# Optimization experiments

Measured on AMD Instinct MI355X. Metric: run time of the kernel, lower is better.

## Reference

```python
import jax, jax.numpy as jnp
import numpy as np

# --- constants mirroring init_kwargs ---
DIM = 1024
N_HEADS = 16
N_KV_HEADS = 4
HEAD_DIM = DIM // N_HEADS          # 64
REP = N_HEADS // N_KV_HEADS        # 4
ROPE_THETA = 10000.0
WINDOW = 512
N_GLOBAL = 64
EPS = 1e-6


def setup_inputs() -> dict:
    key = jax.random.key(0)
    ks = jax.random.split(key, 7)
    B, L = 2, 2048
    x = jax.random.normal(ks[0], (B, L, DIM), dtype=jnp.float32)
    s = 0.02
    wq = jax.random.normal(ks[1], (DIM, N_HEADS * HEAD_DIM), dtype=jnp.float32) * s
    wk = jax.random.normal(ks[2], (DIM, N_KV_HEADS * HEAD_DIM), dtype=jnp.float32) * s
    wv = jax.random.normal(ks[3], (DIM, N_KV_HEADS * HEAD_DIM), dtype=jnp.float32) * s
    wo = jax.random.normal(ks[4], (N_HEADS * HEAD_DIM, DIM), dtype=jnp.float32) * s
    gq = jnp.ones((HEAD_DIM,), dtype=jnp.float32) + 0.01 * jax.random.normal(ks[5], (HEAD_DIM,), dtype=jnp.float32)
    gk = jnp.ones((HEAD_DIM,), dtype=jnp.float32) + 0.01 * jax.random.normal(ks[6], (HEAD_DIM,), dtype=jnp.float32)
    return {"x": x, "wq": wq, "wk": wk, "wv": wv, "wo": wo, "gq": gq, "gk": gk}


def _rmsnorm(t, g):
    # QKNorm: RMS norm over head_dim with learnable per-dim scale
    return t * jax.lax.rsqrt(jnp.mean(t * t, axis=-1, keepdims=True) + EPS) * g


def _rope(t, cos, sin):
    # t: [B,H,L,hd]; complex RoPE over consecutive pairs (2i, 2i+1)
    t1 = t[..., 0::2]
    t2 = t[..., 1::2]
    o1 = t1 * cos - t2 * sin
    o2 = t1 * sin + t2 * cos
    return jnp.stack([o1, o2], axis=-1).reshape(t.shape)


def reference(x, wq, wk, wv, wo, gq, gk):
    B, L, D = x.shape
    q = (x @ wq).reshape(B, L, N_HEADS, HEAD_DIM)
    k = (x @ wk).reshape(B, L, N_KV_HEADS, HEAD_DIM)
    v = (x @ wv).reshape(B, L, N_KV_HEADS, HEAD_DIM)
    q = _rmsnorm(q, gq)
    k = _rmsnorm(k, gk)
    q = q.transpose(0, 2, 1, 3)  # [B,H,L,hd]
    k = k.transpose(0, 2, 1, 3)
    v = v.transpose(0, 2, 1, 3)

    # RoPE frequencies (start_pos = 0)
    inv_freq = 1.0 / (ROPE_THETA ** (jnp.arange(0, HEAD_DIM, 2, dtype=jnp.float32) / HEAD_DIM))
    ang = jnp.arange(L, dtype=jnp.float32)[:, None] * inv_freq[None, :]  # [L, hd/2]
    cos, sin = jnp.cos(ang), jnp.sin(ang)
    q = _rope(q, cos, sin)
    k = _rope(k, cos, sin)

    # GQA: repeat kv heads (repeat_interleave on head dim)
    k = jnp.repeat(k, REP, axis=1)
    v = jnp.repeat(v, REP, axis=1)

    scores = jnp.einsum("bhqd,bhkd->bhqk", q, k) / np.sqrt(HEAD_DIM).astype(np.float32)

    # sliding-window + global-token causal mask
    half = WINDOW // 2
    i = jnp.arange(L)[:, None]
    j = jnp.arange(L)[None, :]
    m = (j <= i) & ((j >= i - half) | (j < N_GLOBAL))  # [L,L] bool
    scores = jnp.where(m[None, None], scores, -jnp.inf)

    attn = jax.nn.softmax(scores.astype(jnp.float32), axis=-1).astype(scores.dtype)
    out = jnp.einsum("bhqk,bhkd->bhqd", attn, v)
    out = out.transpose(0, 2, 1, 3).reshape(B, L, N_HEADS * HEAD_DIM)
    return out @ wo
```

## Files before the change

kernel.cpp:

```cpp
#include <hip/hip_runtime.h>
#include <hip/hip_bf16.h>

typedef __bf16 bf16x8 __attribute__((ext_vector_type(8)));
typedef __bf16 bf16x4 __attribute__((ext_vector_type(4)));
typedef float  f32x4  __attribute__((ext_vector_type(4)));
typedef short  s16x4  __attribute__((ext_vector_type(4)));

__device__ __forceinline__ __bf16 to_bf16(float f) {
    __hip_bfloat16 h = __float2bfloat16(f);
    return *reinterpret_cast<__bf16*>(&h);
}

__device__ __forceinline__ f32x4 mfma32(bf16x8 a, bf16x8 b, f32x4 c) {
    return __builtin_amdgcn_mfma_f32_16x16x32_bf16(a, b, c, 0, 0, 0);
}
__device__ __forceinline__ f32x4 mfma16(bf16x4 a, bf16x4 b, f32x4 c) {
#if __has_builtin(__builtin_amdgcn_mfma_f32_16x16x16_bf16)
    return __builtin_amdgcn_mfma_f32_16x16x16_bf16(a, b, c, 0, 0, 0);
#else
    return __builtin_amdgcn_mfma_f32_16x16x16bf16_1k(
        __builtin_bit_cast(s16x4, a), __builtin_bit_cast(s16x4, b), c, 0, 0, 0);
#endif
}

__device__ __forceinline__ void gload_lds16(const __bf16* g, __bf16* l) {
    __builtin_amdgcn_global_load_lds(
        (const __attribute__((address_space(1))) void*)g,
        (__attribute__((address_space(3))) void*)l, 16, 0, 0);
}


__global__ __launch_bounds__(256) void prep_k(const float* __restrict__ wq,
                                              const float* __restrict__ wk,
                                              const float* __restrict__ wv,
                                              __bf16* __restrict__ WqkvT,
                                              float2* __restrict__ rope_tab) {
    int b = blockIdx.x, tid = threadIdx.x;
    if (b >= 1536) {
        int idx = (b - 1536) * 256 + tid;
        int pos = idx >> 5, f = idx & 31;
        float ex = (float)(2 * f) * (1.0f / 64.0f);
        float invf = expf(-ex * 9.210340371976184f);
        float ang = (float)pos * invf;
        rope_tab[idx] = make_float2(cosf(ang), sinf(ang));
        return;
    }
    __shared__ float tile[32][36];
    const float* src; __bf16* dst; int N, idx;
    if (b < 1024)      { src = wq; dst = WqkvT;                        N = 1024; idx = b; }
    else if (b < 1280) { src = wk; dst = WqkvT + (size_t)1024 * 1024;  N = 256;  idx = b - 1024; }
    else               { src = wv; dst = WqkvT + (size_t)1280 * 1024;  N = 256;  idx = b - 1280; }
    int k0 = (idx & 31) * 32, n0 = (idx >> 5) * 32;
    int row = tid >> 3, c4 = tid & 7;
    *(f32x4*)&tile[row][c4 * 4] = *(const f32x4*)(src + (size_t)(k0 + row) * N + n0 + c4 * 4);
    __syncthreads();
    bf16x4 v;
#pragma unroll
    for (int j = 0; j < 4; ++j) v[j] = to_bf16(tile[c4 * 4 + j][row]);
    *(bf16x4*)&dst[(size_t)(n0 + row) * 1024 + k0 + c4 * 4] = v;
}

__global__ __launch_bounds__(512, 4) void gemmqkv_k(const float* __restrict__ X,
                                                    const __bf16* __restrict__ BT,
                                                    const float2* __restrict__ rope_tab,
                                                    const float* __restrict__ gq,
                                                    const float* __restrict__ gk,
                                                    const float* __restrict__ wo,
                                                    __bf16* __restrict__ Qb,
                                                    __bf16* __restrict__ Kbl,
                                                    __bf16* __restrict__ Vt,
                                                    __bf16* __restrict__ WoT) {
    extern __shared__ char smem_raw[];
    int tid = threadIdx.x;
    if (blockIdx.y >= 12) {
        float* scr = (float*)smem_raw;
        int bidT = (blockIdx.y - 12) * 32 + blockIdx.x;
        int sub = tid >> 8, t8 = tid & 255;
        int row = t8 >> 3, c4 = t8 & 7;
        float* my = scr + sub * 1152;
#pragma unroll
        for (int r = 0; r < 4; ++r) {
            int tile = bidT * 8 + r * 2 + sub;
            int k0 = (tile & 31) * 32, n0t = (tile >> 5) * 32;
            __syncthreads();
            *(f32x4*)&my[row * 36 + c4 * 4] =
                *(const f32x4*)(wo + (size_t)(k0 + row) * 1024 + n0t + c4 * 4);
            __syncthreads();
            bf16x4 v;
#pragma unroll
            for (int j = 0; j < 4; ++j) v[j] = to_bf16(my[(c4 * 4 + j) * 36 + row]);
            *(bf16x4*)&WoT[(size_t)(n0t + row) * 1024 + k0 + c4 * 4] = v;
        }
        return;
    }
    __shared__ float ssp[4][128];
    __bf16* smem = (__bf16*)smem_raw;
    int m0 = blockIdx.x * 128, n0 = blockIdx.y * 128;
    int wid = tid >> 6, lane = tid & 63;
    int wm = (wid & 1) * 64, wn = (wid >> 1) * 32;
    int lm = lane & 15, qd = lane >> 4;
    int arow = tid >> 3, aslot = tid & 7;
    int asrc = aslot ^ (arow & 7);
    f32x4 acc[4][2] = {};
    f32x4 areg[4];

    auto A_LOAD = [&](int t) {
        const float* ap = X + (size_t)(m0 + arow) * 1024 + t * 64 + asrc * 8;
        areg[0] = *(const f32x4*)ap;
        areg[1] = *(const f32x4*)(ap + 4);
        const float* ap2 = ap + (size_t)64 * 1024;
        areg[2] = *(const f32x4*)ap2;
        areg[3] = *(const f32x4*)(ap2 + 4);
    };
    auto A_WRITE = [&](int bsel) {
        __bf16* ab = smem + bsel * 16384;
        bf16x8 w0, w1;
#pragma unroll
        for (int j = 0; j < 4; ++j) {
            w0[j] = to_bf16(areg[0][j]); w0[4 + j] = to_bf16(areg[1][j]);
            w1[j] = to_bf16(areg[2][j]); w1[4 + j] = to_bf16(areg[3][j]);
        }
        *(bf16x8*)&ab[arow * 64 + aslot * 8] = w0;
        *(bf16x8*)&ab[(arow + 64) * 64 + aslot * 8] = w1;
    };
    auto B_GLOAD = [&](int bsel, int t) {
        __bf16* base = smem + bsel * 16384 + 8192;
#pragma unroll
        for (int r = 0; r < 2; ++r) {
            int row = r * 64 + (tid >> 3);
            int c8 = (tid & 7) ^ (row & 7);
            gload_lds16(BT + (size_t)(n0 + row) * 1024 + t * 64 + c8 * 8,
                        base + r * 4096 + wid * 512);
        }
    };

    A_LOAD(0);
    B_GLOAD(0, 0);
    asm volatile("s_waitcnt vmcnt(2)" ::: "memory");
    A_WRITE(0);

    for (int t = 0; t < 16; ++t) {
        if (t + 1 < 16) {
            A_LOAD(t + 1);
            B_GLOAD((t + 1) & 1, t + 1);
            asm volatile("s_waitcnt vmcnt(6)" ::: "memory");
        } else {
            asm volatile("s_waitcnt vmcnt(0)" ::: "memory");
        }
        asm volatile("s_waitcnt lgkmcnt(0)" ::: "memory");
        __builtin_amdgcn_s_barrier();
        __builtin_amdgcn_sched_barrier(0);
        const __bf16* cA = smem + (t & 1) * 16384;
        const __bf16* cB = cA + 8192;
#pragma unroll
        for (int kh = 0; kh < 2; ++kh) {
            bf16x8 af[4], bfr[2];
#pragma unroll
            for (int t4 = 0; t4 < 4; ++t4) {
                int row = wm + t4 * 16 + lm;
                af[t4] = *(const bf16x8*)&cA[row * 64 + (((kh * 4 + qd) ^ (row & 7)) * 8)];
            }
#pragma unroll
            for (int j = 0; j < 2; ++j) {
                int col = wn + j * 16 + lm;
                bfr[j] = *(const bf16x8*)&cB[col * 64 + (((kh * 4 + qd) ^ (col & 7)) * 8)];
            }
#pragma unroll
            for (int ti = 0; ti < 4; ++ti)
#pragma unroll
                for (int tj = 0; tj < 2; ++tj)
                    acc[ti][tj] = mfma32(af[ti], bfr[tj], acc[ti][tj]);
        }
        if (t + 1 < 16) {
            asm volatile("s_waitcnt vmcnt(2)" ::: "memory");
            A_WRITE((t + 1) & 1);
        }
        asm volatile("s_waitcnt lgkmcnt(0)" ::: "memory");
        __builtin_amdgcn_s_barrier();
    }

    int head0 = n0 >> 6;
    int quad = wid >> 1;
    int chead = wn & 63;

    if (head0 < 20) {
        int head = head0 + (quad >> 1);
        bool isq = head < 16;
        const float* gvec = isq ? gq : gk;
        float gam[2];
#pragma unroll
        for (int tj = 0; tj < 2; ++tj) gam[tj] = gvec[chead + tj * 16 + lm];

#pragma unroll
        for (int ti = 0; ti < 4; ++ti)
#pragma unroll
            for (int r = 0; r < 4; ++r) {
                float sq = acc[ti][0][r] * acc[ti][0][r] + acc[ti][1][r] * acc[ti][1][r];
                sq += __shfl_xor(sq, 1);
                sq += __shfl_xor(sq, 2);
                sq += __shfl_xor(sq, 4);
                sq += __shfl_xor(sq, 8);
                if (lm == 0) ssp[quad][wm + ti * 16 + qd * 4 + r] = sq;
            }
        __syncthreads();

#pragma unroll
        for (int ti = 0; ti < 4; ++ti)
#pragma unroll
            for (int r = 0; r < 4; ++r) {
                int row = wm + ti * 16 + qd * 4 + r;
                int t = m0 + row;
                int pos = t & 2047, bb = t >> 11;
                float ss = ssp[quad][row] + ssp[quad ^ 1][row];
                float scale = rsqrtf(ss * (1.0f / 64.0f) + 1e-6f);
#pragma unroll
                for (int tj = 0; tj < 2; ++tj) {
                    int cw = chead + tj * 16 + lm;
                    float v = acc[ti][tj][r] * scale * gam[tj];
                    float2 cs = rope_tab[pos * 32 + (cw >> 1)];
                    float pv = __shfl_xor(v, 1);
                    float outv = (cw & 1) ? (pv * cs.y + v * cs.x) : (v * cs.x - pv * cs.y);
                    if (isq) {
                        int kvh = head >> 2, h4 = head & 3;
                        size_t off = (((((size_t)bb * 4 + kvh) * 128 + (pos >> 4)) * 4 + h4) * 16
                                      + (pos & 15)) * 64 + cw;
                        Qb[off] = to_bf16(outv * 0.125f);
                    } else {
                        int kvg = head - 16;
                        Kbl[(((size_t)bb * 4 + kvg) * 2048 + pos) * 64 + cw] = to_bf16(outv);
                    }
                }
            }
    } else {
        __bf16* tvh = smem + (quad >> 1) * 8704;
        int bb = m0 >> 11, pos0 = m0 & 2047;
#pragma unroll
        for (int ti = 0; ti < 4; ++ti)
#pragma unroll
            for (int tj = 0; tj < 2; ++tj)
#pragma unroll
                for (int r = 0; r < 4; ++r) {
                    int row = wm + ti * 16 + qd * 4 + r;
                    int cw = chead + tj * 16 + lm;
                    tvh[cw * 136 + row] = to_bf16(acc[ti][tj][r]);
                }
        __syncthreads();
        int hh = tid >> 8, t8 = tid & 255;
        int kvg = head0 + hh - 20;
        size_t gg = (size_t)bb * 4 + kvg;
        const __bf16* tvr = smem + hh * 8704;
#pragma unroll
        for (int p = 0; p < 4; ++p) {
            int d = p * 16 + (t8 >> 4);
            int tok = (t8 & 15) * 8;
            bf16x8 vvv = *(const bf16x8*)&tvr[d * 136 + tok];
            *(bf16x8*)(Vt + (gg * 64 + d) * 2048 + pos0 + tok) = vvv;
        }
    }
}

__global__ __launch_bounds__(512, 4) void gemm_op_k(const __bf16* __restrict__ A,
                                                    const __bf16* __restrict__ BT,
                                                    float* __restrict__ C) {
    extern __shared__ char smem_raw[];
    __bf16* smem = (__bf16*)smem_raw;
    int tid = threadIdx.x;
    int m0 = blockIdx.x * 128, n0 = blockIdx.y * 64;
    int wid = tid >> 6, lane = tid & 63;
    int wm = (wid & 3) * 32, wn = (wid >> 2) * 32;
    int lm = lane & 15, qd = lane >> 4;
    f32x4 acc[2][2] = {};
    auto STAGE = [&](int bsel, int t) {
        __bf16* base = smem + bsel * 12288;
#pragma unroll
        for (int r = 0; r < 2; ++r) {
            int row = r * 64 + (tid >> 3);
            int c8 = (tid & 7) ^ (row & 7);
            gload_lds16(A + (size_t)(m0 + row) * 1024 + t * 64 + c8 * 8,
                        base + r * 4096 + wid * 512);
        }
        {
            int row = tid >> 3;
            int c8 = (tid & 7) ^ (row & 7);
            gload_lds16(BT + (size_t)(n0 + row) * 1024 + t * 64 + c8 * 8,
                        base + 8192 + wid * 512);
        }
    };
    STAGE(0, 0);
    for (int t = 0; t < 16; ++t) {
        if (t + 1 < 16) {
            STAGE((t + 1) & 1, t + 1);
            asm volatile("s_waitcnt vmcnt(3)" ::: "memory");
        } else {
            asm volatile("s_waitcnt vmcnt(0)" ::: "memory");
        }
        __builtin_amdgcn_s_barrier();
        __builtin_amdgcn_sched_barrier(0);
        const __bf16* cA = smem + (t & 1) * 12288;
        const __bf16* cB = cA + 8192;
#pragma unroll
        for (int kh = 0; kh < 2; ++kh) {
            bf16x8 af[2], bfr[2];
#pragma unroll
            for (int i = 0; i < 2; ++i) {
                int row = wm + i * 16 + lm;
                af[i] = *(const bf16x8*)&cA[row * 64 + (((kh * 4 + qd) ^ (row & 7)) * 8)];
                int col = wn + i * 16 + lm;
                bfr[i] = *(const bf16x8*)&cB[col * 64 + (((kh * 4 + qd) ^ (col & 7)) * 8)];
            }
#pragma unroll
            for (int ti = 0; ti < 2; ++ti)
#pragma unroll
                for (int tj = 0; tj < 2; ++tj)
                    acc[ti][tj] = mfma32(af[ti], bfr[tj], acc[ti][tj]);
        }
        asm volatile("s_waitcnt lgkmcnt(0)" ::: "memory");
        __builtin_amdgcn_s_barrier();
    }
#pragma unroll
    for (int ti = 0; ti < 2; ++ti)
#pragma unroll
        for (int tj = 0; tj < 2; ++tj)
#pragma unroll
            for (int r = 0; r < 4; ++r) {
                int row = m0 + wm + ti * 16 + qd * 4 + r;
                int col = n0 + wn + tj * 16 + lm;
                C[(size_t)row * 1024 + col] = acc[ti][tj][r];
            }
}

__global__ __launch_bounds__(512, 4) void attn_k(const __bf16* __restrict__ Qb,
                                                 const __bf16* __restrict__ Kbl,
                                                 const __bf16* __restrict__ Vt,
                                                 __bf16* __restrict__ aout) {
    __shared__ __bf16 Kt[2][64 * 64];
    __shared__ __bf16 Vl[2][64 * 64];
    int tid = threadIdx.x, wid = tid >> 6, lane = tid & 63;
    int l15 = lane & 15, quad = lane >> 4;
    int qb = blockIdx.x, kvh = blockIdx.y, b = blockIdx.z;
    int qg = wid >> 2;
    int h4 = wid & 3;
    int iw0 = qb * 32;
    int iw = iw0 + qg * 16;
    int g = b * 4 + kvh;
    int h = kvh * 4 + h4;
    int e7 = l15 & 7;

    int qbi = qb * 2 + qg;
    const __bf16* qp = Qb + ((((size_t)g * 128 + qbi) * 4 + h4) * 16 + l15) * 64 + quad * 8;
    bf16x8 qf0 = *(const bf16x8*)qp;
    bf16x8 qf1 = *(const bf16x8*)(qp + 32);

    int ts = (iw0 - 256) >> 6; if (ts < 1) ts = 1;
    int tmaxb = (iw0 + 31) >> 6;
    int n_all = (tmaxb >= ts) ? (tmaxb - ts + 2) : 1;
    int tmaxw = (iw + 15) >> 6;

    const __bf16* Kg = Kbl + (size_t)g * 2048 * 64;
    const __bf16* Vg = Vt + (size_t)g * 64 * 2048;

    int r0 = tid >> 3, c0 = tid & 7;
    int kl = r0 * 64 + ((c0 ^ (r0 & 7)) * 8);

    bf16x8 kr, vr;
    auto stage_load = [&](int tt) {
        kr = *(const bf16x8*)(Kg + (size_t)tt * 64 * 64 + r0 * 64 + c0 * 8);
        vr = *(const bf16x8*)(Vg + (size_t)r0 * 2048 + tt * 64 + c0 * 8);
    };
    auto stage_write = [&](int buf) {
        *(bf16x8*)&Kt[buf][kl] = kr;
        *(bf16x8*)&Vl[buf][kl] = vr;
    };

    stage_load(0);
    stage_write(0);

    f32x4 o[4] = {};
    float mr = -1e30f, lrp = 0.f;
    int iq = iw + l15;

    for (int idx = 0; idx < n_all; ++idx) {
        int tt = (idx == 0) ? 0 : ts + idx - 1;
        if (idx + 1 < n_all) stage_load(ts + idx);
        __syncthreads();
        int buf = idx & 1;

        f32x4 s[4] = {};
#pragma unroll
        for (int nt = 0; nt < 4; ++nt) {
            const __bf16* kp = &Kt[buf][(nt * 16 + l15) * 64];
            bf16x8 k0 = *(const bf16x8*)(kp + ((quad ^ e7) * 8));
            bf16x8 k1 = *(const bf16x8*)(kp + (((quad + 4) ^ e7) * 8));
            s[nt] = mfma32(k0, qf0, s[nt]);
            s[nt] = mfma32(k1, qf1, s[nt]);
        }

        bool need_mask = (tt >= tmaxw) || (tt >= 1 && tt * 64 < iw + 15 - 256);
        if (need_mask) {
#pragma unroll
            for (int nt = 0; nt < 4; ++nt)
#pragma unroll
                for (int r = 0; r < 4; ++r) {
                    int j = tt * 64 + nt * 16 + quad * 4 + r;
                    bool valid = (j <= iq) && ((j >= iq - 256) || (j < 64));
                    s[nt][r] = valid ? s[nt][r] : -1e30f;
                }
        }

        float mx = -1e30f;
#pragma unroll
        for (int nt = 0; nt < 4; ++nt)
#pragma unroll
            for (int r = 0; r < 4; ++r) mx = fmaxf(mx, s[nt][r]);
        mx = fmaxf(mx, __shfl_xor(mx, 16));
        mx = fmaxf(mx, __shfl_xor(mx, 32));
        float mn = fmaxf(mr, mx);
        float alpha = __expf(mr - mn);
        mr = mn;

        float ps = 0.f;
        bf16x4 pb[4];
#pragma unroll
        for (int nt = 0; nt < 4; ++nt)
#pragma unroll
            for (int r = 0; r < 4; ++r) {
                float pv = __expf(s[nt][r] - mn);
                ps += pv;
                pb[nt][r] = to_bf16(pv);
            }
        lrp = lrp * alpha + ps;

#pragma unroll
        for (int dt = 0; dt < 4; ++dt) {
            o[dt] *= alpha;
            const __bf16* vp = &Vl[buf][(dt * 16 + l15) * 64];
#pragma unroll
            for (int nt = 0; nt < 4; ++nt) {
                int c8 = 2 * nt + (quad >> 1);
                bf16x4 va = *(const bf16x4*)(vp + ((c8 ^ e7) * 8) + (quad & 1) * 4);
                o[dt] = mfma16(va, pb[nt], o[dt]);
            }
        }

        if (idx + 1 < n_all) stage_write((idx + 1) & 1);
    }

    lrp += __shfl_xor(lrp, 16);
    lrp += __shfl_xor(lrp, 32);
    float inv = 1.f / lrp;
    __syncthreads();
    __bf16* pr = (__bf16*)Kt + wid * 16 * 64;
#pragma unroll
    for (int dt = 0; dt < 4; ++dt)
#pragma unroll
        for (int r = 0; r < 4; ++r) {
            int e = dt * 16 + quad * 4 + r;
            int c8 = e >> 3;
            pr[l15 * 64 + ((c8 ^ e7) * 8) + (e & 7)] = to_bf16(o[dt][r] * inv);
        }
    bf16x8 o0 = *(const bf16x8*)(pr + l15 * 64 + (((2 * quad) ^ e7) * 8));
    bf16x8 o1 = *(const bf16x8*)(pr + l15 * 64 + (((2 * quad + 1) ^ e7) * 8));
    __bf16* op = aout + ((size_t)b * 2048 + iw + l15) * 1024 + h * 64 + quad * 16;
    *(bf16x8*)op = o0;
    *(bf16x8*)(op + 8) = o1;
}

extern "C" void kernel_launch(void* const* d_in, const int* in_sizes, int n_in,
                              void* d_out, int out_size, void* d_ws, size_t ws_size,
                              hipStream_t stream) {
    const float* x  = (const float*)d_in[0];
    const float* wq = (const float*)d_in[1];
    const float* wk = (const float*)d_in[2];
    const float* wv = (const float*)d_in[3];
    const float* wo = (const float*)d_in[4];
    const float* gq = (const float*)d_in[5];
    const float* gk = (const float*)d_in[6];
    float* out = (float*)d_out;

    char* ws = (char*)d_ws;
    __bf16*  WqkvT = (__bf16*)ws;
    __bf16*  WoT   = (__bf16*)(ws + 3145728);
    __bf16*  aout  = (__bf16*)(ws + 5242880);
    __bf16*  Kbl   = (__bf16*)(ws + 13631488);
    __bf16*  Vt    = (__bf16*)(ws + 15728640);
    __bf16*  Qb    = (__bf16*)(ws + 17825792);
    float2*  rtab  = (float2*)(ws + 26214400);

    prep_k<<<1792, dim3(256), 0, stream>>>(wq, wk, wv, WqkvT, rtab);
    gemmqkv_k<<<dim3(32, 16), dim3(512), 65536, stream>>>(x, WqkvT, rtab, gq, gk, wo,
                                                          Qb, Kbl, Vt, WoT);
    attn_k<<<dim3(64, 4, 2), dim3(512), 0, stream>>>(Qb, Kbl, Vt, aout);
    gemm_op_k<<<dim3(32, 16), dim3(512), 49152, stream>>>(aout, WoT, out);
}
```

Measured before the change: 138.3 us.

## Fuse all four stages into one persistent cooperative kernel with grid syncs

Replaces four separate kernel launches (weight prep, QKV GEMM, attention, output projection) with a single cooperative persistent kernel. Each block loops over work items of each stage, and grid-wide syncs separate the stages. This removes launch overhead and inter-kernel gaps. In exchange, occupancy is capped by the largest shared-memory stage, grid syncs add cost, and work distribution changes when the grid has fewer blocks than the old per-stage grids.

Measured after the change: 413.8 us. 2.99x slower.

```diff
diff --git a/kernel.cpp b/kernel.cpp
--- a/kernel.cpp
+++ b/kernel.cpp
@@ -1,10 +1,12 @@
 #include <hip/hip_runtime.h>
+#include <hip/hip_cooperative_groups.h>
 #include <hip/hip_bf16.h>
+
+namespace cg = cooperative_groups;
 
 typedef __bf16 bf16x8 __attribute__((ext_vector_type(8)));
 typedef __bf16 bf16x4 __attribute__((ext_vector_type(4)));
 typedef float  f32x4  __attribute__((ext_vector_type(4)));
-typedef short  s16x4  __attribute__((ext_vector_type(4)));
 
 __device__ __forceinline__ __bf16 to_bf16(float f) {
     __hip_bfloat16 h = __float2bfloat16(f);
@@ -18,6 +20,7 @@
 #if __has_builtin(__builtin_amdgcn_mfma_f32_16x16x16_bf16)
     return __builtin_amdgcn_mfma_f32_16x16x16_bf16(a, b, c, 0, 0, 0);
 #else
+    typedef short s16x4 __attribute__((ext_vector_type(4)));
     return __builtin_amdgcn_mfma_f32_16x16x16bf16_1k(
         __builtin_bit_cast(s16x4, a), __builtin_bit_cast(s16x4, b), c, 0, 0, 0);
 #endif
@@ -30,439 +33,422 @@
 }
 
 
-__global__ __launch_bounds__(256) void prep_k(const float* __restrict__ wq,
-                                              const float* __restrict__ wk,
-                                              const float* __restrict__ wv,
-                                              __bf16* __restrict__ WqkvT,
-                                              float2* __restrict__ rope_tab) {
-    int b = blockIdx.x, tid = threadIdx.x;
-    if (b >= 1536) {
-        int idx = (b - 1536) * 256 + tid;
-        int pos = idx >> 5, f = idx & 31;
-        float ex = (float)(2 * f) * (1.0f / 64.0f);
-        float invf = expf(-ex * 9.210340371976184f);
-        float ang = (float)pos * invf;
-        rope_tab[idx] = make_float2(cosf(ang), sinf(ang));
-        return;
-    }
-    __shared__ float tile[32][36];
-    const float* src; __bf16* dst; int N, idx;
-    if (b < 1024)      { src = wq; dst = WqkvT;                        N = 1024; idx = b; }
-    else if (b < 1280) { src = wk; dst = WqkvT + (size_t)1024 * 1024;  N = 256;  idx = b - 1024; }
-    else               { src = wv; dst = WqkvT + (size_t)1280 * 1024;  N = 256;  idx = b - 1280; }
-    int k0 = (idx & 31) * 32, n0 = (idx >> 5) * 32;
-    int row = tid >> 3, c4 = tid & 7;
-    *(f32x4*)&tile[row][c4 * 4] = *(const f32x4*)(src + (size_t)(k0 + row) * N + n0 + c4 * 4);
-    __syncthreads();
-    bf16x4 v;
-#pragma unroll
-    for (int j = 0; j < 4; ++j) v[j] = to_bf16(tile[c4 * 4 + j][row]);
-    *(bf16x4*)&dst[(size_t)(n0 + row) * 1024 + k0 + c4 * 4] = v;
-}
-
-__global__ __launch_bounds__(512, 4) void gemmqkv_k(const float* __restrict__ X,
-                                                    const __bf16* __restrict__ BT,
-                                                    const float2* __restrict__ rope_tab,
-                                                    const float* __restrict__ gq,
-                                                    const float* __restrict__ gk,
-                                                    const float* __restrict__ wo,
-                                                    __bf16* __restrict__ Qb,
-                                                    __bf16* __restrict__ Kbl,
-                                                    __bf16* __restrict__ Vt,
-                                                    __bf16* __restrict__ WoT) {
+__global__ __launch_bounds__(512, 4) void fused_k(
+        const float* __restrict__ X,  const float* __restrict__ wq,
+        const float* __restrict__ wk, const float* __restrict__ wv,
+        const float* __restrict__ wo, const float* __restrict__ gq,
+        const float* __restrict__ gk,
+        __bf16* __restrict__ WqkvT, __bf16* __restrict__ WoT,
+        float2* __restrict__ rtab,
+        __bf16* __restrict__ Qb, __bf16* __restrict__ Kbl,
+        __bf16* __restrict__ Vt, __bf16* __restrict__ aout,
+        float* __restrict__ out) {
     extern __shared__ char smem_raw[];
-    int tid = threadIdx.x;
-    if (blockIdx.y >= 12) {
+    __shared__ float ssp[4][128];
+    cg::grid_group gg = cg::this_grid();
+    const int tid = threadIdx.x;
+    const int nb = gridDim.x;
+
+    {
         float* scr = (float*)smem_raw;
-        int bidT = (blockIdx.y - 12) * 32 + blockIdx.x;
         int sub = tid >> 8, t8 = tid & 255;
         int row = t8 >> 3, c4 = t8 & 7;
         float* my = scr + sub * 1152;
-#pragma unroll
-        for (int r = 0; r < 4; ++r) {
-            int tile = bidT * 8 + r * 2 + sub;
-            int k0 = (tile & 31) * 32, n0t = (tile >> 5) * 32;
+        for (int base2 = blockIdx.x * 2; base2 < 2560; base2 += nb * 2) {
+            int tile = base2 + sub;
+            const float* src = wq; __bf16* dst = WqkvT; int N = 1024; int idx = tile;
+            if (tile >= 1536)      { src = wo; dst = WoT;                       N = 1024; idx = tile - 1536; }
+            else if (tile >= 1280) { src = wv; dst = WqkvT + (size_t)1280*1024; N = 256;  idx = tile - 1280; }
+            else if (tile >= 1024) { src = wk; dst = WqkvT + (size_t)1024*1024; N = 256;  idx = tile - 1024; }
+            int k0 = (idx & 31) * 32, n0 = (idx >> 5) * 32;
             __syncthreads();
             *(f32x4*)&my[row * 36 + c4 * 4] =
-                *(const f32x4*)(wo + (size_t)(k0 + row) * 1024 + n0t + c4 * 4);
+                *(const f32x4*)(src + (size_t)(k0 + row) * N + n0 + c4 * 4);
             __syncthreads();
             bf16x4 v;
 #pragma unroll
             for (int j = 0; j < 4; ++j) v[j] = to_bf16(my[(c4 * 4 + j) * 36 + row]);
-            *(bf16x4*)&WoT[(size_t)(n0t + row) * 1024 + k0 + c4 * 4] = v;
-        }
-        return;
+            *(bf16x4*)&dst[(size_t)(n0 + row) * 1024 + k0 + c4 * 4] = v;
+        }
+        for (int gid = blockIdx.x * 512 + tid; gid < 65536; gid += nb * 512) {
+            int pos = gid >> 5, f = gid & 31;
+            float ex = (float)(2 * f) * (1.0f / 64.0f);
+            float invf = expf(-ex * 9.210340371976184f);
+            float ang = (float)pos * invf;
+            rtab[gid] = make_float2(cosf(ang), sinf(ang));
+        }
     }
-    __shared__ float ssp[4][128];
-    __bf16* smem = (__bf16*)smem_raw;
-    int m0 = blockIdx.x * 128, n0 = blockIdx.y * 128;
-    int wid = tid >> 6, lane = tid & 63;
-    int wm = (wid & 1) * 64, wn = (wid >> 1) * 32;
-    int lm = lane & 15, qd = lane >> 4;
-    int arow = tid >> 3, aslot = tid & 7;
-    int asrc = aslot ^ (arow & 7);
-    f32x4 acc[4][2] = {};
-    f32x4 areg[4];
-
-    auto A_LOAD = [&](int t) {
-        const float* ap = X + (size_t)(m0 + arow) * 1024 + t * 64 + asrc * 8;
-        areg[0] = *(const f32x4*)ap;
-        areg[1] = *(const f32x4*)(ap + 4);
-        const float* ap2 = ap + (size_t)64 * 1024;
-        areg[2] = *(const f32x4*)ap2;
-        areg[3] = *(const f32x4*)(ap2 + 4);
-    };
-    auto A_WRITE = [&](int bsel) {
-        __bf16* ab = smem + bsel * 16384;
-        bf16x8 w0, w1;
-#pragma unroll
-        for (int j = 0; j < 4; ++j) {
-            w0[j] = to_bf16(areg[0][j]); w0[4 + j] = to_bf16(areg[1][j]);
-            w1[j] = to_bf16(areg[2][j]); w1[4 + j] = to_bf16(areg[3][j]);
-        }
-        *(bf16x8*)&ab[arow * 64 + aslot * 8] = w0;
-        *(bf16x8*)&ab[(arow + 64) * 64 + aslot * 8] = w1;
-    };
-    auto B_GLOAD = [&](int bsel, int t) {
-        __bf16* base = smem + bsel * 16384 + 8192;
-#pragma unroll
-        for (int r = 0; r < 2; ++r) {
-            int row = r * 64 + (tid >> 3);
-            int c8 = (tid & 7) ^ (row & 7);
-            gload_lds16(BT + (size_t)(n0 + row) * 1024 + t * 64 + c8 * 8,
-                        base + r * 4096 + wid * 512);
-        }
-    };
-
-    A_LOAD(0);
-    B_GLOAD(0, 0);
-    asm volatile("s_waitcnt vmcnt(2)" ::: "memory");
-    A_WRITE(0);
-
-    for (int t = 0; t < 16; ++t) {
-        if (t + 1 < 16) {
-            A_LOAD(t + 1);
-            B_GLOAD((t + 1) & 1, t + 1);
-            asm volatile("s_waitcnt vmcnt(6)" ::: "memory");
-        } else {
-            asm volatile("s_waitcnt vmcnt(0)" ::: "memory");
-        }
-        asm volatile("s_waitcnt lgkmcnt(0)" ::: "memory");
-        __builtin_amdgcn_s_barrier();
-        __builtin_amdgcn_sched_barrier(0);
-        const __bf16* cA = smem + (t & 1) * 16384;
-        const __bf16* cB = cA + 8192;
-#pragma unroll
-        for (int kh = 0; kh < 2; ++kh) {
-            bf16x8 af[4], bfr[2];
-#pragma unroll
-            for (int t4 = 0; t4 < 4; ++t4) {
-                int row = wm + t4 * 16 + lm;
-                af[t4] = *(const bf16x8*)&cA[row * 64 + (((kh * 4 + qd) ^ (row & 7)) * 8)];
-            }
-#pragma unroll
-            for (int j = 0; j < 2; ++j) {
-                int col = wn + j * 16 + lm;
-                bfr[j] = *(const bf16x8*)&cB[col * 64 + (((kh * 4 + qd) ^ (col & 7)) * 8)];
-            }
+    __threadfence();
+    gg.sync();
+
+    for (int wb = blockIdx.x; wb < 384; wb += nb) {
+        __bf16* smem = (__bf16*)smem_raw;
+        int m0 = (wb & 31) * 128, n0 = (wb >> 5) * 128;
+        int wid = tid >> 6, lane = tid & 63;
+        int wm = (wid & 1) * 64, wn = (wid >> 1) * 32;
+        int lm = lane & 15, qd = lane >> 4;
+        int arow = tid >> 3, aslot = tid & 7;
+        int asrc = aslot ^ (arow & 7);
+        f32x4 acc[4][2] = {};
+        f32x4 areg[4];
+
+        auto A_LOAD = [&](int t) {
+            const float* ap = X + (size_t)(m0 + arow) * 1024 + t * 64 + asrc * 8;
+            areg[0] = *(const f32x4*)ap;
+            areg[1] = *(const f32x4*)(ap + 4);
+            const float* ap2 = ap + (size_t)64 * 1024;
+            areg[2] = *(const f32x4*)ap2;
+            areg[3] = *(const f32x4*)(ap2 + 4);
+        };
+        auto A_WRITE = [&](int bsel) {
+            __bf16* ab = smem + bsel * 16384;
+            bf16x8 w0, w1;
+#pragma unroll
+            for (int j = 0; j < 4; ++j) {
+                w0[j] = to_bf16(areg[0][j]); w0[4 + j] = to_bf16(areg[1][j]);
+                w1[j] = to_bf16(areg[2][j]); w1[4 + j] = to_bf16(areg[3][j]);
+            }
+            *(bf16x8*)&ab[arow * 64 + aslot * 8] = w0;
+            *(bf16x8*)&ab[(arow + 64) * 64 + aslot * 8] = w1;
+        };
+        auto B_GLOAD = [&](int bsel, int t) {
+            __bf16* base = smem + bsel * 16384 + 8192;
+#pragma unroll
+            for (int r = 0; r < 2; ++r) {
+                int row = r * 64 + (tid >> 3);
+                int c8 = (tid & 7) ^ (row & 7);
+                gload_lds16(WqkvT + (size_t)(n0 + row) * 1024 + t * 64 + c8 * 8,
+                            base + r * 4096 + wid * 512);
+            }
+        };
+
+        A_LOAD(0);
+        B_GLOAD(0, 0);
+        asm volatile("s_waitcnt vmcnt(2)" ::: "memory");
+        A_WRITE(0);
+
+        for (int t = 0; t < 16; ++t) {
+            if (t + 1 < 16) {
+                A_LOAD(t + 1);
+                B_GLOAD((t + 1) & 1, t + 1);
+                asm volatile("s_waitcnt vmcnt(6)" ::: "memory");
+            } else {
+                asm volatile("s_waitcnt vmcnt(0)" ::: "memory");
+            }
+            asm volatile("s_waitcnt lgkmcnt(0)" ::: "memory");
+            __builtin_amdgcn_s_barrier();
+            __builtin_amdgcn_sched_barrier(0);
+            const __bf16* cA = smem + (t & 1) * 16384;
+            const __bf16* cB = cA + 8192;
+#pragma unroll
+            for (int kh = 0; kh < 2; ++kh) {
+                bf16x8 af[4], bfr[2];
+#pragma unroll
+                for (int t4 = 0; t4 < 4; ++t4) {
+                    int row = wm + t4 * 16 + lm;
+                    af[t4] = *(const bf16x8*)&cA[row * 64 + (((kh * 4 + qd) ^ (row & 7)) * 8)];
+                }
+#pragma unroll
+                for (int j = 0; j < 2; ++j) {
+                    int col = wn + j * 16 + lm;
+                    bfr[j] = *(const bf16x8*)&cB[col * 64 + (((kh * 4 + qd) ^ (col & 7)) * 8)];
+                }
+#pragma unroll
+                for (int ti = 0; ti < 4; ++ti)
+#pragma unroll
+                    for (int tj = 0; tj < 2; ++tj)
+                        acc[ti][tj] = mfma32(af[ti], bfr[tj], acc[ti][tj]);
+            }
+            if (t + 1 < 16) {
+                asm volatile("s_waitcnt vmcnt(2)" ::: "memory");
+                A_WRITE((t + 1) & 1);
+            }
+            asm volatile("s_waitcnt lgkmcnt(0)" ::: "memory");
+            __builtin_amdgcn_s_barrier();
+        }
+
+        int head0 = n0 >> 6;
+        int quad = wid >> 1;
+        int chead = wn & 63;
+
+        if (head0 < 20) {
+            int head = head0 + (quad >> 1);
+            bool isq = head < 16;
+            const float* gvec = isq ? gq : gk;
+            float gam[2];
+#pragma unroll
+            for (int tj = 0; tj < 2; ++tj) gam[tj] = gvec[chead + tj * 16 + lm];
 #pragma unroll
             for (int ti = 0; ti < 4; ++ti)
 #pragma unroll
-                for (int tj = 0; tj < 2; ++tj)
-                    acc[ti][tj] = mfma32(af[ti], bfr[tj], acc[ti][tj]);
-        }
-        if (t + 1 < 16) {
-            asm volatile("s_waitcnt vmcnt(2)" ::: "memory");
-            A_WRITE((t + 1) & 1);
-        }
-        asm volatile("s_waitcnt lgkmcnt(0)" ::: "memory");
-        __builtin_amdgcn_s_barrier();
-    }
-
-    int head0 = n0 >> 6;
-    int quad = wid >> 1;
-    int chead = wn & 63;
-
-    if (head0 < 20) {
-        int head = head0 + (quad >> 1);
-        bool isq = head < 16;
-        const float* gvec = isq ? gq : gk;
-        float gam[2];
-#pragma unroll
-        for (int tj = 0; tj < 2; ++tj) gam[tj] = gvec[chead + tj * 16 + lm];
-
-#pragma unroll
-        for (int ti = 0; ti < 4; ++ti)
-#pragma unroll
-            for (int r = 0; r < 4; ++r) {
-                float sq = acc[ti][0][r] * acc[ti][0][r] + acc[ti][1][r] * acc[ti][1][r];
-                sq += __shfl_xor(sq, 1);
-                sq += __shfl_xor(sq, 2);
-                sq += __shfl_xor(sq, 4);
-                sq += __shfl_xor(sq, 8);
-                if (lm == 0) ssp[quad][wm + ti * 16 + qd * 4 + r] = sq;
-            }
-        __syncthreads();
-
-#pragma unroll
-        for (int ti = 0; ti < 4; ++ti)
-#pragma unroll
-            for (int r = 0; r < 4; ++r) {
-                int row = wm + ti * 16 + qd * 4 + r;
-                int t = m0 + row;
-                int pos = t & 2047, bb = t >> 11;
-                float ss = ssp[quad][row] + ssp[quad ^ 1][row];
-                float scale = rsqrtf(ss * (1.0f / 64.0f) + 1e-6f);
-#pragma unroll
-                for (int tj = 0; tj < 2; ++tj) {
-                    int cw = chead + tj * 16 + lm;
-                    float v = acc[ti][tj][r] * scale * gam[tj];
-                    float2 cs = rope_tab[pos * 32 + (cw >> 1)];
-                    float pv = __shfl_xor(v, 1);
-                    float outv = (cw & 1) ? (pv * cs.y + v * cs.x) : (v * cs.x - pv * cs.y);
-                    if (isq) {
-                        int kvh = head >> 2, h4 = head & 3;
-                        size_t off = (((((size_t)bb * 4 + kvh) * 128 + (pos >> 4)) * 4 + h4) * 16
-                                      + (pos & 15)) * 64 + cw;
-                        Qb[off] = to_bf16(outv * 0.125f);
-                    } else {
-                        int kvg = head - 16;
-                        Kbl[(((size_t)bb * 4 + kvg) * 2048 + pos) * 64 + cw] = to_bf16(outv);
-                    }
-                }
-            }
-    } else {
-        __bf16* tvh = smem + (quad >> 1) * 8704;
-        int bb = m0 >> 11, pos0 = m0 & 2047;
-#pragma unroll
-        for (int ti = 0; ti < 4; ++ti)
-#pragma unroll
-            for (int tj = 0; tj < 2; ++tj)
+                for (int r = 0; r < 4; ++r) {
+                    float sq = acc[ti][0][r] * acc[ti][0][r] + acc[ti][1][r] * acc[ti][1][r];
+                    sq += __shfl_xor(sq, 1);
+                    sq += __shfl_xor(sq, 2);
+                    sq += __shfl_xor(sq, 4);
+                    sq += __shfl_xor(sq, 8);
+                    if (lm == 0) ssp[quad][wm + ti * 16 + qd * 4 + r] = sq;
+                }
+            __syncthreads();
+#pragma unroll
+            for (int ti = 0; ti < 4; ++ti)
 #pragma unroll
                 for (int r = 0; r < 4; ++r) {
                     int row = wm + ti * 16 + qd * 4 + r;
-                    int cw = chead + tj * 16 + lm;
-                    tvh[cw * 136 + row] = to_bf16(acc[ti][tj][r]);
-                }
+                    int t = m0 + row;
+                    int pos = t & 2047, bb = t >> 11;
+                    float ss = ssp[quad][row] + ssp[quad ^ 1][row];
+                    float scale = rsqrtf(ss * (1.0f / 64.0f) + 1e-6f);
+#pragma unroll
+                    for (int tj = 0; tj < 2; ++tj) {
+                        int cw = chead + tj * 16 + lm;
+                        float v = acc[ti][tj][r] * scale * gam[tj];
+                        float2 cs = rtab[pos * 32 + (cw >> 1)];
+                        float pv = __shfl_xor(v, 1);
+                        float outv = (cw & 1) ? (pv * cs.y + v * cs.x) : (v * cs.x - pv * cs.y);
+                        if (isq) {
+                            int kvh = head >> 2, h4 = head & 3;
+                            size_t off = (((((size_t)bb * 4 + kvh) * 128 + (pos >> 4)) * 4 + h4) * 16
+                                          + (pos & 15)) * 64 + cw;
+                            Qb[off] = to_bf16(outv * 0.125f);
+                        } else {
+                            int kvg = head - 16;
+                            Kbl[(((size_t)bb * 4 + kvg) * 2048 + pos) * 64 + cw] = to_bf16(outv);
+                        }
+                    }
+                }
+            __syncthreads();
+        } else {
+            __bf16* tvh = smem + (quad >> 1) * 8704;
+            int bb = m0 >> 11, pos0 = m0 & 2047;
+#pragma unroll
+            for (int ti = 0; ti < 4; ++ti)
+#pragma unroll
+                for (int tj = 0; tj < 2; ++tj)
+#pragma unroll
+                    for (int r = 0; r < 4; ++r) {
+                        int row = wm + ti * 16 + qd * 4 + r;
+                        int cw = chead + tj * 16 + lm;
+                        tvh[cw * 136 + row] = to_bf16(acc[ti][tj][r]);
+                    }
+            __syncthreads();
+            int hh = tid >> 8, t8 = tid & 255;
+            int kvg = head0 + hh - 20;
+            size_t gg2 = (size_t)bb * 4 + kvg;
+            const __bf16* tvr = smem + hh * 8704;
+#pragma unroll
+            for (int p = 0; p < 4; ++p) {
+                int d = p * 16 + (t8 >> 4);
+                int tok = (t8 & 15) * 8;
+                bf16x8 vvv = *(const bf16x8*)&tvr[d * 136 + tok];
+                *(bf16x8*)(Vt + (gg2 * 64 + d) * 2048 + pos0 + tok) = vvv;
+            }
+            __syncthreads();
+        }
+    }
+    __threadfence();
+    gg.sync();
+
+    for (int wb = blockIdx.x; wb < 512; wb += nb) {
+        __bf16* smem = (__bf16*)smem_raw;
+        int wid = tid >> 6, lane = tid & 63;
+        int l15 = lane & 15, quad = lane >> 4;
+        int qb = wb & 63, kvh = (wb >> 6) & 3, b = wb >> 8;
+        int qg = wid >> 2;
+        int h4 = wid & 3;
+        int iw0 = qb * 32;
+        int iw = iw0 + qg * 16;
+        int g = b * 4 + kvh;
+        int h = kvh * 4 + h4;
+        int e7 = l15 & 7;
+
+        int qbi = qb * 2 + qg;
+        const __bf16* qp = Qb + ((((size_t)g * 128 + qbi) * 4 + h4) * 16 + l15) * 64 + quad * 8;
+        bf16x8 qf0 = *(const bf16x8*)qp;
+        bf16x8 qf1 = *(const bf16x8*)(qp + 32);
+
+        int ts = (iw0 - 256) >> 6; if (ts < 1) ts = 1;
+        int tmaxb = (iw0 + 31) >> 6;
+        int n_all = (tmaxb >= ts) ? (tmaxb - ts + 2) : 1;
+        int tmaxw = (iw + 15) >> 6;
+
+        const __bf16* Kg = Kbl + (size_t)g * 2048 * 64;
+        const __bf16* Vg = Vt + (size_t)g * 64 * 2048;
+
+        int r0 = tid >> 3, c0 = tid & 7;
+        int kl = r0 * 64 + ((c0 ^ (r0 & 7)) * 8);
+
+        bf16x8 kr, vr;
+        auto stage_load = [&](int tt) {
+            kr = *(const bf16x8*)(Kg + (size_t)tt * 64 * 64 + r0 * 64 + c0 * 8);
+            vr = *(const bf16x8*)(Vg + (size_t)r0 * 2048 + tt * 64 + c0 * 8);
+        };
+        auto stage_write = [&](int buf) {
+            *(bf16x8*)&smem[buf * 4096 + kl] = kr;
+            *(bf16x8*)&smem[8192 + buf * 4096 + kl] = vr;
+        };
+
+        stage_load(0);
+        stage_write(0);
+
+        f32x4 o[4] = {};
+        float mr = -1e30f, lrp = 0.f;
+        int iq = iw + l15;
+
+        for (int idx = 0; idx < n_all; ++idx) {
+            int tt = (idx == 0) ? 0 : ts + idx - 1;
+            if (idx + 1 < n_all) stage_load(ts + idx);
+            __syncthreads();
+            int buf = idx & 1;
+
+            f32x4 s[4] = {};
+#pragma unroll
+            for (int nt = 0; nt < 4; ++nt) {
+                const __bf16* kp = &smem[buf * 4096 + (nt * 16 + l15) * 64];
+                bf16x8 k0 = *(const bf16x8*)(kp + ((quad ^ e7) * 8));
+                bf16x8 k1 = *(const bf16x8*)(kp + (((quad + 4) ^ e7) * 8));
+                s[nt] = mfma32(k0, qf0, s[nt]);
+                s[nt] = mfma32(k1, qf1, s[nt]);
+            }
+
+            bool need_mask = (tt >= tmaxw) || (tt >= 1 && tt * 64 < iw + 15 - 256);
+            if (need_mask) {
+#pragma unroll
+                for (int nt = 0; nt < 4; ++nt)
+#pragma unroll
+                    for (int r = 0; r < 4; ++r) {
+                        int j = tt * 64 + nt * 16 + quad * 4 + r;
+                        bool valid = (j <= iq) && ((j >= iq - 256) || (j < 64));
+                        s[nt][r] = valid ? s[nt][r] : -1e30f;
+                    }
+            }
+
+            float mx = -1e30f;
+#pragma unroll
+            for (int nt = 0; nt < 4; ++nt)
+#pragma unroll
+                for (int r = 0; r < 4; ++r) mx = fmaxf(mx, s[nt][r]);
+            mx = fmaxf(mx, __shfl_xor(mx, 16));
+            mx = fmaxf(mx, __shfl_xor(mx, 32));
+            float mn = fmaxf(mr, mx);
+            float alpha = __expf(mr - mn);
+            mr = mn;
+
+            float ps = 0.f;
+            bf16x4 pb[4];
+#pragma unroll
+            for (int nt = 0; nt < 4; ++nt)
+#pragma unroll
+                for (int r = 0; r < 4; ++r) {
+                    float pv = __expf(s[nt][r] - mn);
+                    ps += pv;
+                    pb[nt][r] = to_bf16(pv);
+                }
+            lrp = lrp * alpha + ps;
+
+#pragma unroll
+            for (int dt = 0; dt < 4; ++dt) {
+                o[dt] *= alpha;
+                const __bf16* vp = &smem[8192 + buf * 4096 + (dt * 16 + l15) * 64];
+#pragma unroll
+                for (int nt = 0; nt < 4; ++nt) {
+                    int c8 = 2 * nt + (quad >> 1);
+                    bf16x4 va = *(const bf16x4*)(vp + ((c8 ^ e7) * 8) + (quad & 1) * 4);
+                    o[dt] = mfma16(va, pb[nt], o[dt]);
+                }
+            }
+
+            if (idx + 1 < n_all) stage_write((idx + 1) & 1);
+        }
+
+        lrp += __shfl_xor(lrp, 16);
+        lrp += __shfl_xor(lrp, 32);
+        float inv = 1.f / lrp;
         __syncthreads();
-        int hh = tid >> 8, t8 = tid & 255;
-        int kvg = head0 + hh - 20;
-        size_t gg = (size_t)bb * 4 + kvg;
-        const __bf16* tvr = smem + hh * 8704;
-#pragma unroll
-        for (int p = 0; p < 4; ++p) {
-            int d = p * 16 + (t8 >> 4);
-            int tok = (t8 & 15) * 8;
-            bf16x8 vvv = *(const bf16x8*)&tvr[d * 136 + tok];
-            *(bf16x8*)(Vt + (gg * 64 + d) * 2048 + pos0 + tok) = vvv;
-        }
+        __bf16* pr = smem + wid * 1024;
+#pragma unroll
+        for (int dt = 0; dt < 4; ++dt)
+#pragma unroll
+            for (int r = 0; r < 4; ++r) {
+                int e = dt * 16 + quad * 4 + r;
+                int c8 = e >> 3;
+                pr[l15 * 64 + ((c8 ^ e7) * 8) + (e & 7)] = to_bf16(o[dt][r] * inv);
+            }
+        bf16x8 o0 = *(const bf16x8*)(pr + l15 * 64 + (((2 * quad) ^ e7) * 8));
+        bf16x8 o1 = *(const bf16x8*)(pr + l15 * 64 + (((2 * quad + 1) ^ e7) * 8));
+        __bf16* op = aout + ((size_t)b * 2048 + iw + l15) * 1024 + h * 64 + quad * 16;
+        *(bf16x8*)op = o0;
+        *(bf16x8*)(op + 8) = o1;
+        __syncthreads();
     }
-}
-
-__global__ __launch_bounds__(512, 4) void gemm_op_k(const __bf16* __restrict__ A,
-                                                    const __bf16* __restrict__ BT,
-                                                    float* __restrict__ C) {
-    extern __shared__ char smem_raw[];
-    __bf16* smem = (__bf16*)smem_raw;
-    int tid = threadIdx.x;
-    int m0 = blockIdx.x * 128, n0 = blockIdx.y * 64;
-    int wid = tid >> 6, lane = tid & 63;
-    int wm = (wid & 3) * 32, wn = (wid >> 2) * 32;
-    int lm = lane & 15, qd = lane >> 4;
-    f32x4 acc[2][2] = {};
-    auto STAGE = [&](int bsel, int t) {
-        __bf16* base = smem + bsel * 12288;
-#pragma unroll
-        for (int r = 0; r < 2; ++r) {
-            int row = r * 64 + (tid >> 3);
-            int c8 = (tid & 7) ^ (row & 7);
-            gload_lds16(A + (size_t)(m0 + row) * 1024 + t * 64 + c8 * 8,
-                        base + r * 4096 + wid * 512);
-        }
-        {
-            int row = tid >> 3;
-            int c8 = (tid & 7) ^ (row & 7);
-            gload_lds16(BT + (size_t)(n0 + row) * 1024 + t * 64 + c8 * 8,
-                        base + 8192 + wid * 512);
-        }
-    };
-    STAGE(0, 0);
-    for (int t = 0; t < 16; ++t) {
-        if (t + 1 < 16) {
-            STAGE((t + 1) & 1, t + 1);
-            asm volatile("s_waitcnt vmcnt(3)" ::: "memory");
-        } else {
-            asm volatile("s_waitcnt vmcnt(0)" ::: "memory");
-        }
-        __builtin_amdgcn_s_barrier();
-        __builtin_amdgcn_sched_barrier(0);
-        const __bf16* cA = smem + (t & 1) * 12288;
-        const __bf16* cB = cA + 8192;
-#pragma unroll
-        for (int kh = 0; kh < 2; ++kh) {
-            bf16x8 af[2], bfr[2];
-#pragma unroll
-            for (int i = 0; i < 2; ++i) {
-                int row = wm + i * 16 + lm;
-                af[i] = *(const bf16x8*)&cA[row * 64 + (((kh * 4 + qd) ^ (row & 7)) * 8)];
-                int col = wn + i * 16 + lm;
-                bfr[i] = *(const bf16x8*)&cB[col * 64 + (((kh * 4 + qd) ^ (col & 7)) * 8)];
-            }
-#pragma unroll
-            for (int ti = 0; ti < 2; ++ti)
-#pragma unroll
-                for (int tj = 0; tj < 2; ++tj)
-                    acc[ti][tj] = mfma32(af[ti], bfr[tj], acc[ti][tj]);
-        }
-        asm volatile("s_waitcnt lgkmcnt(0)" ::: "memory");
-        __builtin_amdgcn_s_barrier();
+    __threadfence();
+    gg.sync();
+
+    for (int wb = blockIdx.x; wb < 512; wb += nb) {
+        __bf16* smem = (__bf16*)smem_raw;
+        int m0 = (wb & 31) * 128, n0 = (wb >> 5) * 64;
+        int wid = tid >> 6, lane = tid & 63;
+        int wm = (wid & 3) * 32, wn = (wid >> 2) * 32;
+        int lm = lane & 15, qd = lane >> 4;
+        f32x4 acc[2][2] = {};
+        auto STAGE = [&](int bsel, int t) {
+            __bf16* base = smem + bsel * 12288;
+#pragma unroll
+            for (int r = 0; r < 2; ++r) {
+                int row = r * 64 + (tid >> 3);
+                int c8 = (tid & 7) ^ (row & 7);
+                gload_lds16(aout + (size_t)(m0 + row) * 1024 + t * 64 + c8 * 8,
+                            base + r * 4096 + wid * 512);
+            }
+            {
+                int row = tid >> 3;
+                int c8 = (tid & 7) ^ (row & 7);
+                gload_lds16(WoT + (size_t)(n0 + row) * 1024 + t * 64 + c8 * 8,
+                            base + 8192 + wid * 512);
+            }
+        };
+        STAGE(0, 0);
+        for (int t = 0; t < 16; ++t) {
+            if (t + 1 < 16) {
+                STAGE((t + 1) & 1, t + 1);
+                asm volatile("s_waitcnt vmcnt(3)" ::: "memory");
+            } else {
+                asm volatile("s_waitcnt vmcnt(0)" ::: "memory");
+            }
+            __builtin_amdgcn_s_barrier();
+            __builtin_amdgcn_sched_barrier(0);
+            const __bf16* cA = smem + (t & 1) * 12288;
+            const __bf16* cB = cA + 8192;
+#pragma unroll
+            for (int kh = 0; kh < 2; ++kh) {
+                bf16x8 af[2], bfr[2];
+#pragma unroll
+                for (int i = 0; i < 2; ++i) {
+                    int row = wm + i * 16 + lm;
+                    af[i] = *(const bf16x8*)&cA[row * 64 + (((kh * 4 + qd) ^ (row & 7)) * 8)];
+                    int col = wn + i * 16 + lm;
+                    bfr[i] = *(const bf16x8*)&cB[col * 64 + (((kh * 4 + qd) ^ (col & 7)) * 8)];
+                }
+#pragma unroll
+                for (int ti = 0; ti < 2; ++ti)
+#pragma unroll
+                    for (int tj = 0; tj < 2; ++tj)
+                        acc[ti][tj] = mfma32(af[ti], bfr[tj], acc[ti][tj]);
+            }
+            asm volatile("s_waitcnt lgkmcnt(0)" ::: "memory");
+            __builtin_amdgcn_s_barrier();
+        }
+#pragma unroll
+        for (int ti = 0; ti < 2; ++ti)
+#pragma unroll
+            for (int tj = 0; tj < 2; ++tj)
+#pragma unroll
+                for (int r = 0; r < 4; ++r) {
+                    int row = m0 + wm + ti * 16 + qd * 4 + r;
+                    int col = n0 + wn + tj * 16 + lm;
+                    out[(size_t)row * 1024 + col] = acc[ti][tj][r];
+                }
     }
-#pragma unroll
-    for (int ti = 0; ti < 2; ++ti)
-#pragma unroll
-        for (int tj = 0; tj < 2; ++tj)
-#pragma unroll
-            for (int r = 0; r < 4; ++r) {
-                int row = m0 + wm + ti * 16 + qd * 4 + r;
-                int col = n0 + wn + tj * 16 + lm;
-                C[(size_t)row * 1024 + col] = acc[ti][tj][r];
-            }
-}
-
-__global__ __launch_bounds__(512, 4) void attn_k(const __bf16* __restrict__ Qb,
-                                                 const __bf16* __restrict__ Kbl,
-                                                 const __bf16* __restrict__ Vt,
-                                                 __bf16* __restrict__ aout) {
-    __shared__ __bf16 Kt[2][64 * 64];
-    __shared__ __bf16 Vl[2][64 * 64];
-    int tid = threadIdx.x, wid = tid >> 6, lane = tid & 63;
-    int l15 = lane & 15, quad = lane >> 4;
-    int qb = blockIdx.x, kvh = blockIdx.y, b = blockIdx.z;
-    int qg = wid >> 2;
-    int h4 = wid & 3;
-    int iw0 = qb * 32;
-    int iw = iw0 + qg * 16;
-    int g = b * 4 + kvh;
-    int h = kvh * 4 + h4;
-    int e7 = l15 & 7;
-
-    int qbi = qb * 2 + qg;
-    const __bf16* qp = Qb + ((((size_t)g * 128 + qbi) * 4 + h4) * 16 + l15) * 64 + quad * 8;
-    bf16x8 qf0 = *(const bf16x8*)qp;
-    bf16x8 qf1 = *(const bf16x8*)(qp + 32);
-
-    int ts = (iw0 - 256) >> 6; if (ts < 1) ts = 1;
-    int tmaxb = (iw0 + 31) >> 6;
-    int n_all = (tmaxb >= ts) ? (tmaxb - ts + 2) : 1;
-    int tmaxw = (iw + 15) >> 6;
-
-    const __bf16* Kg = Kbl + (size_t)g * 2048 * 64;
-    const __bf16* Vg = Vt + (size_t)g * 64 * 2048;
-
-    int r0 = tid >> 3, c0 = tid & 7;
-    int kl = r0 * 64 + ((c0 ^ (r0 & 7)) * 8);
-
-    bf16x8 kr, vr;
-    auto stage_load = [&](int tt) {
-        kr = *(const bf16x8*)(Kg + (size_t)tt * 64 * 64 + r0 * 64 + c0 * 8);
-        vr = *(const bf16x8*)(Vg + (size_t)r0 * 2048 + tt * 64 + c0 * 8);
-    };
-    auto stage_write = [&](int buf) {
-        *(bf16x8*)&Kt[buf][kl] = kr;
-        *(bf16x8*)&Vl[buf][kl] = vr;
-    };
-
-    stage_load(0);
-    stage_write(0);
-
-    f32x4 o[4] = {};
-    float mr = -1e30f, lrp = 0.f;
-    int iq = iw + l15;
-
-    for (int idx = 0; idx < n_all; ++idx) {
-        int tt = (idx == 0) ? 0 : ts + idx - 1;
-        if (idx + 1 < n_all) stage_load(ts + idx);
-        __syncthreads();
-        int buf = idx & 1;
-
-        f32x4 s[4] = {};
-#pragma unroll
-        for (int nt = 0; nt < 4; ++nt) {
-            const __bf16* kp = &Kt[buf][(nt * 16 + l15) * 64];
-            bf16x8 k0 = *(const bf16x8*)(kp + ((quad ^ e7) * 8));
-            bf16x8 k1 = *(const bf16x8*)(kp + (((quad + 4) ^ e7) * 8));
-            s[nt] = mfma32(k0, qf0, s[nt]);
-            s[nt] = mfma32(k1, qf1, s[nt]);
-        }
-
-        bool need_mask = (tt >= tmaxw) || (tt >= 1 && tt * 64 < iw + 15 - 256);
-        if (need_mask) {
-#pragma unroll
-            for (int nt = 0; nt < 4; ++nt)
-#pragma unroll
-                for (int r = 0; r < 4; ++r) {
-                    int j = tt * 64 + nt * 16 + quad * 4 + r;
-                    bool valid = (j <= iq) && ((j >= iq - 256) || (j < 64));
-                    s[nt][r] = valid ? s[nt][r] : -1e30f;
-                }
-        }
-
-        float mx = -1e30f;
-#pragma unroll
-        for (int nt = 0; nt < 4; ++nt)
-#pragma unroll
-            for (int r = 0; r < 4; ++r) mx = fmaxf(mx, s[nt][r]);
-        mx = fmaxf(mx, __shfl_xor(mx, 16));
-        mx = fmaxf(mx, __shfl_xor(mx, 32));
-        float mn = fmaxf(mr, mx);
-        float alpha = __expf(mr - mn);
-        mr = mn;
-
-        float ps = 0.f;
-        bf16x4 pb[4];
-#pragma unroll
-        for (int nt = 0; nt < 4; ++nt)
-#pragma unroll
-            for (int r = 0; r < 4; ++r) {
-                float pv = __expf(s[nt][r] - mn);
-                ps += pv;
-                pb[nt][r] = to_bf16(pv);
-            }
-        lrp = lrp * alpha + ps;
-
-#pragma unroll
-        for (int dt = 0; dt < 4; ++dt) {
-            o[dt] *= alpha;
-            const __bf16* vp = &Vl[buf][(dt * 16 + l15) * 64];
-#pragma unroll
-            for (int nt = 0; nt < 4; ++nt) {
-                int c8 = 2 * nt + (quad >> 1);
-                bf16x4 va = *(const bf16x4*)(vp + ((c8 ^ e7) * 8) + (quad & 1) * 4);
-                o[dt] = mfma16(va, pb[nt], o[dt]);
-            }
-        }
-
-        if (idx + 1 < n_all) stage_write((idx + 1) & 1);
-    }
-
-    lrp += __shfl_xor(lrp, 16);
-    lrp += __shfl_xor(lrp, 32);
-    float inv = 1.f / lrp;
-    __syncthreads();
-    __bf16* pr = (__bf16*)Kt + wid * 16 * 64;
-#pragma unroll
-    for (int dt = 0; dt < 4; ++dt)
-#pragma unroll
-        for (int r = 0; r < 4; ++r) {
-            int e = dt * 16 + quad * 4 + r;
-            int c8 = e >> 3;
-            pr[l15 * 64 + ((c8 ^ e7) * 8) + (e & 7)] = to_bf16(o[dt][r] * inv);
-        }
-    bf16x8 o0 = *(const bf16x8*)(pr + l15 * 64 + (((2 * quad) ^ e7) * 8));
-    bf16x8 o1 = *(const bf16x8*)(pr + l15 * 64 + (((2 * quad + 1) ^ e7) * 8));
-    __bf16* op = aout + ((size_t)b * 2048 + iw + l15) * 1024 + h * 64 + quad * 16;
-    *(bf16x8*)op = o0;
-    *(bf16x8*)(op + 8) = o1;
 }
 
 extern "C" void kernel_launch(void* const* d_in, const int* in_sizes, int n_in,
@@ -486,9 +472,23 @@
     __bf16*  Qb    = (__bf16*)(ws + 17825792);
     float2*  rtab  = (float2*)(ws + 26214400);
 
-    prep_k<<<1792, dim3(256), 0, stream>>>(wq, wk, wv, WqkvT, rtab);
-    gemmqkv_k<<<dim3(32, 16), dim3(512), 65536, stream>>>(x, WqkvT, rtab, gq, gk, wo,
-                                                          Qb, Kbl, Vt, WoT);
-    attn_k<<<dim3(64, 4, 2), dim3(512), 0, stream>>>(Qb, Kbl, Vt, aout);
-    gemm_op_k<<<dim3(32, 16), dim3(512), 49152, stream>>>(aout, WoT, out);
-}
+    static int coop_grid = 0;
+    if (coop_grid == 0) {
+        int bpc = 0;
+        hipOccupancyMaxActiveBlocksPerMultiprocessor(&bpc, fused_k, 512, 65536);
+        hipDeviceProp_t props;
+        int dev = 0;
+        hipGetDevice(&dev);
+        hipGetDeviceProperties(&props, dev);
+        long g = (long)bpc * (long)props.multiProcessorCount;
+        if (g < 1) g = 1;
+        if (g > 512) g = 512;
+        coop_grid = (int)g;
+    }
+
+    void* args[] = {(void*)&x, (void*)&wq, (void*)&wk, (void*)&wv, (void*)&wo,
+                    (void*)&gq, (void*)&gk, (void*)&WqkvT, (void*)&WoT, (void*)&rtab,
+                    (void*)&Qb, (void*)&Kbl, (void*)&Vt, (void*)&aout, (void*)&out};
+    hipLaunchCooperativeKernel((void*)fused_k, dim3(coop_grid), dim3(512),
+                               args, 65536, stream);
+}
```
